# Kernel tuning notes

Hardware: AMD Instinct MI355X
Metric: run time of the kernel (lower is better)

## Reference

```python
import jax, jax.numpy as jnp
import numpy as np

N, M, C, MID, K = 131072, 4096, 32, 16, 6
BN_EPS = 1e-5


def _bn(x, g, b, mu, var):
    # eval-mode BatchNorm over channel (last) axis
    return g * (x - mu) * jax.lax.rsqrt(var + BN_EPS) + b


def _block(x, w1, b1, g, b, mu, var, w2, b2):
    # Conv1d(kernel_size=1) stack == per-position linear over channels
    h = jax.nn.relu(_bn(x @ w1.T + b1, g, b, mu, var))
    return h @ w2.T + b2


def _l2norm(x):
    # F.normalize(p=2, dim=channel) with eps=1e-12 clamp
    return x / jnp.maximum(jnp.linalg.norm(x, axis=-1, keepdims=True), 1e-12)


def _forward(sp_fea, sp_xyz, o_p_fea, p_xyz, idx_abs, idx_rel, params):
    (wf1_w, wf1_b, wf_g, wf_b, wf_m, wf_v, wf2_w, wf2_b,
     wx1_w, wx1_b, wx_g, wx_b, wx_m, wx_v, wx2_w, wx2_b,
     m1_w, m1_b, mb_g, mb_b, mb_m, mb_v, m2_w, m2_b) = params
    m = sp_fea.shape[1]
    c = o_p_fea.shape[1]
    # gather each point's K candidate superpoint fea/xyz, center on the point
    c2p_fea = sp_fea[0][idx_abs] - o_p_fea[:, None, :]   # (n, K, C)
    c2p_xyz = sp_xyz[0][idx_abs] - p_xyz[:, None, :]     # (n, K, 3)
    # point MLP: Linear -> BN -> ReLU -> Linear
    p_fea = jax.nn.relu(_bn(o_p_fea @ m1_w.T + m1_b, mb_g, mb_b, mb_m, mb_v)) @ m2_w.T + m2_b  # (n, C)
    w_fea = _block(c2p_fea, wf1_w, wf1_b, wf_g, wf_b, wf_m, wf_v, wf2_w, wf2_b)  # (n, K, C)
    w_xyz = _block(c2p_xyz, wx1_w, wx1_b, wx_g, wx_b, wx_m, wx_v, wx2_w, wx2_b)  # (n, K, C)
    p_fea, w_fea, w_xyz = _l2norm(p_fea), _l2norm(w_fea), _l2norm(w_xyz)
    # bilateral weights over the K candidates
    bi_w = jax.nn.softmax(
        jnp.einsum('nc,nkc->nk', p_fea, w_fea) * jnp.einsum('nc,nkc->nk', p_fea, w_xyz),
        axis=-1)  # (n, K)
    # weighted segment aggregation points -> superpoints
    # (equivalent to building the dense (m, n) association matrix f and matmul)
    ridx = idx_rel.reshape(-1)                                     # (n*K,)
    wsum = jax.ops.segment_sum(bi_w.reshape(-1), ridx, num_segments=m)  # (m,)
    agg_fea = jax.ops.segment_sum((bi_w[..., None] * o_p_fea[:, None, :]).reshape(-1, c), ridx, num_segments=m)
    agg_xyz = jax.ops.segment_sum((bi_w[..., None] * p_xyz[:, None, :]).reshape(-1, 3), ridx, num_segments=m)
    denom = wsum[:, None] + 1e-8
    return (agg_fea / denom)[None], (agg_xyz / denom)[None]  # (1, m, C), (1, m, 3)


def setup_inputs() -> dict:
    key = jax.random.key(0)
    ks = jax.random.split(key, 20)
    f32 = jnp.float32
    idx = jax.random.randint(ks[4], (1, N, K), 0, M, dtype=jnp.int32)
    inp = {
        'sp_fea': jax.random.normal(ks[0], (1, M, C), f32),
        'sp_xyz': jax.random.normal(ks[1], (1, M, 3), f32),
        'o_p_fea': jax.random.normal(ks[2], (N, C), f32),
        'p_xyz': jax.random.normal(ks[3], (N, 3), f32),
        'c2p_idx_abs': idx,
        'c2p_idx': idx,  # bs=1 -> absolute == relative indices
        'cluster_idx': jax.random.randint(ks[5], (N,), 0, M, dtype=jnp.int32),
        'offset': jnp.array([N], dtype=jnp.int32),
        'wf1_w': jax.random.normal(ks[6], (MID, C), f32) * 0.2,
        'wf1_b': jnp.zeros((MID,), f32),
        'wf_bn_g': jnp.ones((MID,), f32),
        'wf_bn_b': jnp.zeros((MID,), f32),
        'wf_bn_m': jax.random.normal(ks[7], (MID,), f32) * 0.1,
        'wf_bn_v': jax.random.uniform(ks[8], (MID,), f32, 0.5, 1.5),
        'wf2_w': jax.random.normal(ks[9], (C, MID), f32) * 0.2,
        'wf2_b': jnp.zeros((C,), f32),
        'wx1_w': jax.random.normal(ks[10], (MID, 3), f32) * 0.2,
        'wx1_b': jnp.zeros((MID,), f32),
        'wx_bn_g': jnp.ones((MID,), f32),
        'wx_bn_b': jnp.zeros((MID,), f32),
        'wx_bn_m': jax.random.normal(ks[11], (MID,), f32) * 0.1,
        'wx_bn_v': jax.random.uniform(ks[12], (MID,), f32, 0.5, 1.5),
        'wx2_w': jax.random.normal(ks[13], (C, MID), f32) * 0.2,
        'wx2_b': jnp.zeros((C,), f32),
        'mlp1_w': jax.random.normal(ks[14], (C, C), f32) * 0.2,
        'mlp1_b': jnp.zeros((C,), f32),
        'mlp_bn_g': jnp.ones((C,), f32),
        'mlp_bn_b': jnp.zeros((C,), f32),
        'mlp_bn_m': jax.random.normal(ks[15], (C,), f32) * 0.1,
        'mlp_bn_v': jax.random.uniform(ks[16], (C,), f32, 0.5, 1.5),
        'mlp2_w': jax.random.normal(ks[17], (C, C), f32) * 0.2,
        'mlp2_b': jnp.zeros((C,), f32),
    }
    return inp


def reference(sp_fea, sp_xyz, o_p_fea, p_xyz, c2p_idx_abs, c2p_idx, cluster_idx, offset,
              wf1_w, wf1_b, wf_bn_g, wf_bn_b, wf_bn_m, wf_bn_v, wf2_w, wf2_b,
              wx1_w, wx1_b, wx_bn_g, wx_bn_b, wx_bn_m, wx_bn_v, wx2_w, wx2_b,
              mlp1_w, mlp1_b, mlp_bn_g, mlp_bn_b, mlp_bn_m, mlp_bn_v, mlp2_w, mlp2_b):
    params = (wf1_w, wf1_b, wf_bn_g, wf_bn_b, wf_bn_m, wf_bn_v, wf2_w, wf2_b,
              wx1_w, wx1_b, wx_bn_g, wx_bn_b, wx_bn_m, wx_bn_v, wx2_w, wx2_b,
              mlp1_w, mlp1_b, mlp_bn_g, mlp_bn_b, mlp_bn_m, mlp_bn_v, mlp2_w, mlp2_b)
    return _forward(sp_fea, sp_xyz, o_p_fea, p_xyz, c2p_idx_abs[0], c2p_idx[0], params)
```

## Files before the change

kernel.cpp:

```cpp
#include <hip/hip_runtime.h>

#define M_ 4096
#define N_ 131072
#define K_ 6
#define C_ 32
#define MID_ 16
#define CAP_ 320
#define CNT_STRIDE 16
#define PB 32

#define OFF_AF 0
#define OFF_AX (M_*MID_)
#define OFF_CB (2*M_*MID_)
#define CB_WF1T 0
#define CB_WX1T 512
#define CB_M1T  576
#define CB_TM   1600
#define CB_QFMT 1632
#define CB_QXMT 2144
#define CB_QF0  2656
#define CB_QX0  2672
#define CB_G2   2688
#define CB_M2TB 3712
#define CB_PBFV 3744
#define CB_PBXV 3776
#define CB_GF   3808
#define CB_GX   4064
#define CB_VF   4320
#define CB_VX   4336
#define CB_SC   4352
#define CB_N    4360
#define OFF_CNT  (OFF_CB + CB_N + 8)
#define OFF_PAIR (OFF_CNT + M_*CNT_STRIDE)

#define BN_EPS 1e-5f

__global__ void prep_kernel(
    const float* __restrict__ sp_fea, const float* __restrict__ sp_xyz,
    const float* __restrict__ wf1_w, const float* __restrict__ wf1_b,
    const float* __restrict__ wf_g, const float* __restrict__ wf_b,
    const float* __restrict__ wf_m, const float* __restrict__ wf_v,
    const float* __restrict__ wf2_w, const float* __restrict__ wf2_b,
    const float* __restrict__ wx1_w, const float* __restrict__ wx1_b,
    const float* __restrict__ wx_g, const float* __restrict__ wx_b,
    const float* __restrict__ wx_m, const float* __restrict__ wx_v,
    const float* __restrict__ wx2_w, const float* __restrict__ wx2_b,
    const float* __restrict__ m1_w, const float* __restrict__ m1_b,
    const float* __restrict__ mb_g, const float* __restrict__ mb_b,
    const float* __restrict__ mb_m, const float* __restrict__ mb_v,
    const float* __restrict__ m2_w, const float* __restrict__ m2_b,
    float* __restrict__ ws)
{
    const int gid = blockIdx.x * blockDim.x + threadIdx.x;

    if (gid < M_) {
        float sp[32];
        #pragma unroll
        for (int q = 0; q < 8; ++q) {
            float4 v = *(const float4*)(sp_fea + gid*32 + 4*q);
            sp[4*q] = v.x; sp[4*q+1] = v.y; sp[4*q+2] = v.z; sp[4*q+3] = v.w;
        }
        #pragma unroll
        for (int j = 0; j < 16; ++j) {
            float s = wf_g[j] * rsqrtf(wf_v[j] + BN_EPS);
            float t = s * wf1_b[j] + wf_b[j] - s * wf_m[j];
            float acc = 0.f;
            #pragma unroll
            for (int c = 0; c < 32; ++c) acc += sp[c] * wf1_w[j*32 + c];
            ws[OFF_AF + gid*16 + j] = s * acc + t;
        }
        float sx0 = sp_xyz[gid*3], sx1 = sp_xyz[gid*3+1], sx2 = sp_xyz[gid*3+2];
        #pragma unroll
        for (int j = 0; j < 16; ++j) {
            float s = wx_g[j] * rsqrtf(wx_v[j] + BN_EPS);
            float t = s * wx1_b[j] + wx_b[j] - s * wx_m[j];
            float acc = sx0*wx1_w[j*3] + sx1*wx1_w[j*3+1] + sx2*wx1_w[j*3+2];
            ws[OFF_AX + gid*16 + j] = s * acc + t;
        }
    }

    if (blockIdx.x == 0) {
        const int t = threadIdx.x;
        float* cb = ws + OFF_CB;

        for (int e = t; e < 512; e += 256) {
            int c = e >> 4, jj = e & 15;
            float s = wf_g[jj] * rsqrtf(wf_v[jj] + BN_EPS);
            cb[CB_WF1T + e] = s * wf1_w[jj*32 + c];
            float aqf = 0.f, aqx = 0.f;
            #pragma unroll
            for (int i = 0; i < 32; ++i) {
                aqf += wf2_w[i*16 + jj] * m2_w[i*32 + c];
                aqx += wx2_w[i*16 + jj] * m2_w[i*32 + c];
            }
            cb[CB_QFMT + e] = aqf;
            cb[CB_QXMT + e] = aqx;
        }
        if (t < 64) {
            int c = t >> 4, jj = t & 15;
            float s = wx_g[jj] * rsqrtf(wx_v[jj] + BN_EPS);
            cb[CB_WX1T + t] = (c < 3) ? s * wx1_w[jj*3 + c] : 0.f;
        }
        for (int e = t; e < 1024; e += 256) {
            int c = e >> 5, i = e & 31;
            float s = mb_g[i] * rsqrtf(mb_v[i] + BN_EPS);
            cb[CB_M1T + e] = s * m1_w[i*32 + c];
            int q = e >> 5, p = e & 31;
            float a = 0.f;
            #pragma unroll
            for (int i2 = 0; i2 < 32; ++i2) a += m2_w[i2*32 + q] * m2_w[i2*32 + p];
            cb[CB_G2 + e] = a;
        }
        if (t < 32) {
            float s = mb_g[t] * rsqrtf(mb_v[t] + BN_EPS);
            cb[CB_TM + t] = s * m1_b[t] + mb_b[t] - s * mb_m[t];
            float a = 0.f, bf = 0.f, bx = 0.f;
            #pragma unroll
            for (int i2 = 0; i2 < 32; ++i2) {
                a  += m2_w[i2*32 + t] * m2_b[i2];
                bf += m2_w[i2*32 + t] * wf2_b[i2];
                bx += m2_w[i2*32 + t] * wx2_b[i2];
            }
            cb[CB_M2TB + t] = a;
            cb[CB_PBFV + t] = bf;
            cb[CB_PBXV + t] = bx;
        }
        if (t < 256) {
            int jj = t >> 4, p = t & 15;
            float accf = 0.f, accx = 0.f;
            #pragma unroll
            for (int i2 = 0; i2 < 32; ++i2) {
                accf += wf2_w[i2*16 + jj] * wf2_w[i2*16 + p];
                accx += wx2_w[i2*16 + jj] * wx2_w[i2*16 + p];
            }
            cb[CB_GF + t] = accf;
            cb[CB_GX + t] = accx;
        }
        if (t < 16) {
            float q0f = 0.f, q0x = 0.f, vf = 0.f, vx = 0.f;
            #pragma unroll
            for (int i2 = 0; i2 < 32; ++i2) {
                q0f += wf2_w[i2*16 + t] * m2_b[i2];
                q0x += wx2_w[i2*16 + t] * m2_b[i2];
                vf  += wf2_w[i2*16 + t] * wf2_b[i2];
                vx  += wx2_w[i2*16 + t] * wx2_b[i2];
            }
            cb[CB_QF0 + t] = q0f;
            cb[CB_QX0 + t] = q0x;
            cb[CB_VF + t] = vf;
            cb[CB_VX + t] = vx;
        }
        if (t == 0) {
            float bbf = 0.f, bbx = 0.f, bb2 = 0.f, pcf = 0.f, pcx = 0.f;
            #pragma unroll
            for (int i2 = 0; i2 < 32; ++i2) {
                bbf += wf2_b[i2]*wf2_b[i2];
                bbx += wx2_b[i2]*wx2_b[i2];
                bb2 += m2_b[i2]*m2_b[i2];
                pcf += m2_b[i2]*wf2_b[i2];
                pcx += m2_b[i2]*wx2_b[i2];
            }
            cb[CB_SC+0] = bbf; cb[CB_SC+1] = bbx; cb[CB_SC+2] = bb2;
            cb[CB_SC+3] = pcf; cb[CB_SC+4] = pcx;
            cb[CB_SC+5] = 0.f; cb[CB_SC+6] = 0.f; cb[CB_SC+7] = 0.f;
        }
    }
}

__global__ __launch_bounds__(256) void fused_kernel(
    const float* __restrict__ o_p_fea, const float* __restrict__ p_xyz,
    const int* __restrict__ idx_abs, float* __restrict__ ws)
{
    __shared__ float cb[CB_N];
    __shared__ float opl[PB*33];
    __shared__ float hpb[PB*36];
    __shared__ float pkl[PB*72];

    const int tid = threadIdx.x;
    const int base = blockIdx.x * PB;
    {
        const float* src = ws + OFF_CB;
        for (int i = tid; i < CB_N; i += 256) cb[i] = src[i];
        #pragma unroll
        for (int u = 0; u < 4; ++u) {
            const int idx = tid + u*256;
            opl[(idx >> 5)*33 + (idx & 31)] = o_p_fea[(size_t)base*32 + idx];
        }
    }
    __syncthreads();

    const int g = tid >> 4;
    const int j = tid & 15;
    const int n0 = base + 2*g;
    const int n1 = n0 + 1;

    float af0=0.f, af1=0.f, h00=0.f, h01=0.f, h10=0.f, h11=0.f;
    #pragma unroll
    for (int c = 0; c < 32; ++c) {
        const float op0 = opl[(2*g)*33 + c];
        const float op1 = opl[(2*g+1)*33 + c];
        const float w   = cb[CB_WF1T + c*16 + j];
        const float m0  = cb[CB_M1T + c*32 + 2*j];
        const float m1v = cb[CB_M1T + c*32 + 2*j + 1];
        af0 += w*op0;  af1 += w*op1;
        h00 += m0*op0; h01 += m1v*op0;
        h10 += m0*op1; h11 += m1v*op1;
    }
    {
        const float tm0 = cb[CB_TM + 2*j], tm1 = cb[CB_TM + 2*j + 1];
        h00 = fmaxf(h00 + tm0, 0.f); h01 = fmaxf(h01 + tm1, 0.f);
        h10 = fmaxf(h10 + tm0, 0.f); h11 = fmaxf(h11 + tm1, 0.f);
    }
    const float wx0 = cb[CB_WX1T + j], wx1v = cb[CB_WX1T + 16 + j], wx2v = cb[CB_WX1T + 32 + j];
    const float ax0 = wx0*p_xyz[n0*3] + wx1v*p_xyz[n0*3+1] + wx2v*p_xyz[n0*3+2];
    const float ax1 = wx0*p_xyz[n1*3] + wx1v*p_xyz[n1*3+1] + wx2v*p_xyz[n1*3+2];

    hpb[(2*g)*36 + 2*j]       = h00;
    hpb[(2*g)*36 + 2*j + 1]   = h01;
    hpb[(2*g+1)*36 + 2*j]     = h10;
    hpb[(2*g+1)*36 + 2*j + 1] = h11;
    __syncthreads();

    const float q0i = cb[CB_QF0 + j], qx0i = cb[CB_QX0 + j];
    float qf0 = q0i, qf1 = q0i, qx0 = qx0i, qx1 = qx0i;
    float t200=0.f, t201=0.f, t210=0.f, t211=0.f;
    #pragma unroll
    for (int q = 0; q < 32; ++q) {
        const float hq0 = hpb[(2*g)*36 + q];
        const float hq1 = hpb[(2*g+1)*36 + q];
        const float wqf = cb[CB_QFMT + q*16 + j];
        const float wqx = cb[CB_QXMT + q*16 + j];
        const float ga  = cb[CB_G2 + q*32 + 2*j];
        const float gb  = cb[CB_G2 + q*32 + 2*j + 1];
        qf0 += wqf*hq0; qf1 += wqf*hq1;
        qx0 += wqx*hq0; qx1 += wqx*hq1;
        t200 += ga*hq0; t201 += gb*hq0;
        t210 += ga*hq1; t211 += gb*hq1;
    }
    const float m2tb0 = 2.f*cb[CB_M2TB + 2*j], m2tb1 = 2.f*cb[CB_M2TB + 2*j + 1];
    const float pbv0 = cb[CB_PBFV + 2*j], pbv1 = cb[CB_PBFV + 2*j + 1];
    const float pxv0 = cb[CB_PBXV + 2*j], pxv1 = cb[CB_PBXV + 2*j + 1];
    float pn20 = h00*(t200 + m2tb0) + h01*(t201 + m2tb1);
    float pn21 = h10*(t210 + m2tb0) + h11*(t211 + m2tb1);
    float pbf0 = h00*pbv0 + h01*pbv1;
    float pbf1 = h10*pbv0 + h11*pbv1;
    float pbx0 = h00*pxv0 + h01*pxv1;
    float pbx1 = h10*pxv0 + h11*pxv1;
    #pragma unroll
    for (int mm = 1; mm < 16; mm <<= 1) {
        pn20 += __shfl_xor(pn20, mm, 16);
        pn21 += __shfl_xor(pn21, mm, 16);
        pbf0 += __shfl_xor(pbf0, mm, 16);
        pbf1 += __shfl_xor(pbf1, mm, 16);
        pbx0 += __shfl_xor(pbx0, mm, 16);
        pbx1 += __shfl_xor(pbx1, mm, 16);
    }
    const float sc2v = cb[CB_SC + 2], sc3v = cb[CB_SC + 3], sc4v = cb[CB_SC + 4];
    const float inv0 = 1.0f / fmaxf(sqrtf(fmaxf(pn20 + sc2v, 0.f)), 1e-12f);
    const float inv1 = 1.0f / fmaxf(sqrtf(fmaxf(pn21 + sc2v, 0.f)), 1e-12f);

    ((float4*)(pkl + (2*g)*72))[j]   = make_float4(af0, ax0, qf0*inv0, qx0*inv0);
    ((float4*)(pkl + (2*g+1)*72))[j] = make_float4(af1, ax1, qf1*inv1, qx1*inv1);
    if (j == 0) {
        pkl[(2*g)*72 + 64]   = (pbf0 + sc3v) * inv0;
        pkl[(2*g)*72 + 65]   = (pbx0 + sc4v) * inv0;
        pkl[(2*g+1)*72 + 64] = (pbf1 + sc3v) * inv1;
        pkl[(2*g+1)*72 + 65] = (pbx1 + sc4v) * inv1;
    }
    __syncthreads();

    const int slot = tid >> 3;
    const int k    = tid & 7;
    const int n    = base + slot;
    const int kc   = (k < K_) ? k : (K_ - 1);
    const int r    = idx_abs[n * K_ + kc];
    const float* pkb = pkl + slot*72;

    float afr[16], axr[16];
    #pragma unroll
    for (int q4 = 0; q4 < 4; ++q4) {
        float4 a = *(const float4*)(ws + OFF_AF + r*16 + 4*q4);
        float4 b = *(const float4*)(ws + OFF_AX + r*16 + 4*q4);
        afr[4*q4] = a.x; afr[4*q4+1] = a.y; afr[4*q4+2] = a.z; afr[4*q4+3] = a.w;
        axr[4*q4] = b.x; axr[4*q4+1] = b.y; axr[4*q4+2] = b.z; axr[4*q4+3] = b.w;
    }

    float hf[16], hx[16];
    float df = 0.f, dx = 0.f, nf2 = 0.f, nx2 = 0.f;
    #pragma unroll
    for (int jj = 0; jj < 16; ++jj) {
        const float4 v4 = ((const float4*)pkb)[jj];
        const float h1 = fmaxf(afr[jj] - v4.x, 0.f);
        const float h2 = fmaxf(axr[jj] - v4.y, 0.f);
        hf[jj] = h1; hx[jj] = h2;
        df  += v4.z * h1;
        dx  += v4.w * h2;
        nf2 += cb[CB_VF + jj] * h1;
        nx2 += cb[CB_VX + jj] * h2;
    }
    const float scbx = pkb[64], scby = pkb[65];

    float nfq = 0.f, nxq = 0.f;
    #pragma unroll
    for (int q = 0; q < 16; ++q) {
        float sf = 0.f, sx = 0.f;
        #pragma unroll
        for (int p4 = 0; p4 < 4; ++p4) {
            const float4 gf = *(const float4*)&cb[CB_GF + q*16 + 4*p4];
            const float4 gx = *(const float4*)&cb[CB_GX + q*16 + 4*p4];
            sf += gf.x*hf[4*p4] + gf.y*hf[4*p4+1] + gf.z*hf[4*p4+2] + gf.w*hf[4*p4+3];
            sx += gx.x*hx[4*p4] + gx.y*hx[4*p4+1] + gx.z*hx[4*p4+2] + gx.w*hx[4*p4+3];
        }
        nfq += hf[q] * sf;
        nxq += hx[q] * sx;
    }
    const float nf = fmaxf(nfq + 2.f*nf2 + cb[CB_SC + 0], 0.f);
    const float nx = fmaxf(nxq + 2.f*nx2 + cb[CB_SC + 1], 0.f);
    const float invf = 1.0f / fmaxf(sqrtf(nf), 1e-12f);
    const float invx = 1.0f / fmaxf(sqrtf(nx), 1e-12f);
    float logit = ((df + scbx) * invf) * ((dx + scby) * invx);
    if (k >= K_) logit = -3.0e38f;

    float mx = logit;
    mx = fmaxf(mx, __shfl_xor(mx, 1));
    mx = fmaxf(mx, __shfl_xor(mx, 2));
    mx = fmaxf(mx, __shfl_xor(mx, 4));
    float ex = __expf(logit - mx);
    float s = ex;
    s += __shfl_xor(s, 1);
    s += __shfl_xor(s, 2);
    s += __shfl_xor(s, 4);
    const float w = ex / s;

    if (k < K_) {
        int*  cnt   = (int*)(ws + OFF_CNT);
        int2* pairs = (int2*)(ws + OFF_PAIR);
        const int pos = atomicAdd(&cnt[r*CNT_STRIDE], 1);
        if (pos < CAP_) {
            pairs[(size_t)r*CAP_ + pos] = make_int2(n, __float_as_int(w));
        }
    }
}

__global__ __launch_bounds__(256) void agg_kernel(
    const float* __restrict__ ws,
    const float* __restrict__ o_p_fea, const float* __restrict__ p_xyz,
    float* __restrict__ out)
{
    __shared__ float red[4][40];

    const int wave = threadIdx.x >> 6;
    const int lane = threadIdx.x & 63;
    const int m = blockIdx.x;
    const int eo = lane >> 5;
    const int c  = lane & 31;

    const int*  cnt   = (const int*)(ws + OFF_CNT);
    const int2* pairs = (const int2*)(ws + OFF_PAIR);

    int cn = cnt[m*CNT_STRIDE];
    if (cn > CAP_) cn = CAP_;
    const int2* pb = pairs + (size_t)m * CAP_;

    float acc = 0.f, wacc = 0.f, xacc = 0.f;
    for (int e2 = (wave*2 + eo)*2; e2 < cn; e2 += 16) {
        const int4 pq = *(const int4*)&pb[e2];
        {
            const int nn  = pq.x;
            const float w = __int_as_float(pq.y);
            acc += w * o_p_fea[(size_t)nn*32 + c];
            if (c == 0) wacc += w;
            if (c < 3)  xacc += w * p_xyz[nn*3 + c];
        }
        if (e2 + 1 < cn) {
            const int nn  = pq.z;
            const float w = __int_as_float(pq.w);
            acc += w * o_p_fea[(size_t)nn*32 + c];
            if (c == 0) wacc += w;
            if (c < 3)  xacc += w * p_xyz[nn*3 + c];
        }
    }
    acc  += __shfl_xor(acc, 32);
    xacc += __shfl_xor(xacc, 32);
    wacc += __shfl_xor(wacc, 32);
    if (eo == 0) {
        red[wave][c] = acc;
        if (c < 3)  red[wave][33 + c] = xacc;
        if (c == 0) red[wave][36] = wacc;
    }
    __syncthreads();

    if (wave == 0 && eo == 0) {
        const float a = red[0][c] + red[1][c] + red[2][c] + red[3][c];
        const float wtot = red[0][36] + red[1][36] + red[2][36] + red[3][36];
        const float denom = wtot + 1e-8f;
        out[m*32 + c] = a / denom;
        if (c < 3) {
            const float x = red[0][33+c] + red[1][33+c] + red[2][33+c] + red[3][33+c];
            out[M_*C_ + m*3 + c] = x / denom;
        }
    }
}

extern "C" void kernel_launch(void* const* d_in, const int* in_sizes, int n_in,
                              void* d_out, int out_size, void* d_ws, size_t ws_size,
                              hipStream_t stream)
{
    const float* sp_fea  = (const float*)d_in[0];
    const float* sp_xyz  = (const float*)d_in[1];
    const float* o_p_fea = (const float*)d_in[2];
    const float* p_xyz   = (const float*)d_in[3];
    const int*   idx_abs = (const int*)d_in[4];
    const float* wf1_w = (const float*)d_in[8];
    const float* wf1_b = (const float*)d_in[9];
    const float* wf_g  = (const float*)d_in[10];
    const float* wf_b  = (const float*)d_in[11];
    const float* wf_m  = (const float*)d_in[12];
    const float* wf_v  = (const float*)d_in[13];
    const float* wf2_w = (const float*)d_in[14];
    const float* wf2_b = (const float*)d_in[15];
    const float* wx1_w = (const float*)d_in[16];
    const float* wx1_b = (const float*)d_in[17];
    const float* wx_g  = (const float*)d_in[18];
    const float* wx_b  = (const float*)d_in[19];
    const float* wx_m  = (const float*)d_in[20];
    const float* wx_v  = (const float*)d_in[21];
    const float* wx2_w = (const float*)d_in[22];
    const float* wx2_b = (const float*)d_in[23];
    const float* m1_w  = (const float*)d_in[24];
    const float* m1_b  = (const float*)d_in[25];
    const float* mb_g  = (const float*)d_in[26];
    const float* mb_b  = (const float*)d_in[27];
    const float* mb_m  = (const float*)d_in[28];
    const float* mb_v  = (const float*)d_in[29];
    const float* m2_w  = (const float*)d_in[30];
    const float* m2_b  = (const float*)d_in[31];

    float* ws = (float*)d_ws;
    float* out = (float*)d_out;

    hipMemsetAsync(ws + OFF_CNT, 0, (size_t)(M_*CNT_STRIDE) * sizeof(int), stream);

    prep_kernel<<<16, 256, 0, stream>>>(
        sp_fea, sp_xyz,
        wf1_w, wf1_b, wf_g, wf_b, wf_m, wf_v, wf2_w, wf2_b,
        wx1_w, wx1_b, wx_g, wx_b, wx_m, wx_v, wx2_w, wx2_b,
        m1_w, m1_b, mb_g, mb_b, mb_m, mb_v, m2_w, m2_b,
        ws);

    fused_kernel<<<N_/PB, 256, 0, stream>>>(o_p_fea, p_xyz, idx_abs, ws);

    agg_kernel<<<M_, 256, 0, stream>>>(ws, o_p_fea, p_xyz, out);
}
```

Measured before the change: 136.2 us.

## Replace Gram quadratic form with Cholesky-factored triangular norm computation

Precomputes a Cholesky factor of the second-layer Gram matrices in the prep kernel and solves for a linear term, so the per-candidate squared norm becomes a sum of squares of an upper-triangular matvec plus a constant. This roughly halves the inner quadratic-form FLOPs and removes the separate linear-term accumulation. It also overlays the shared-memory buffers for point features and the packed per-point data, shrinking LDS use per block at the cost of an extra barrier. The factorization relies on the Gram matrix being positive definite and clamps tiny pivots, which may change numerics slightly.

```diff
diff --git a/kernel.cpp b/kernel.cpp
--- a/kernel.cpp
+++ b/kernel.cpp
@@ -8,6 +8,7 @@
 #define CAP_ 320
 #define CNT_STRIDE 16
 #define PB 32
+#define PKS 68
 
 #define OFF_AF 0
 #define OFF_AX (M_*MID_)
@@ -24,10 +25,10 @@
 #define CB_M2TB 3712
 #define CB_PBFV 3744
 #define CB_PBXV 3776
-#define CB_GF   3808
-#define CB_GX   4064
-#define CB_VF   4320
-#define CB_VX   4336
+#define CB_UF   3808
+#define CB_UX   4064
+#define CB_CF   4320
+#define CB_CX   4336
 #define CB_SC   4352
 #define CB_N    4360
 #define OFF_CNT  (OFF_CB + CB_N + 8)
@@ -80,6 +81,8 @@
     }
 
     if (blockIdx.x == 0) {
+        __shared__ float sG[512];
+        __shared__ float svv[40];
         const int t = threadIdx.x;
         float* cb = ws + OFF_CB;
 
@@ -125,7 +128,7 @@
             cb[CB_PBFV + t] = bf;
             cb[CB_PBXV + t] = bx;
         }
-        if (t < 256) {
+        {
             int jj = t >> 4, p = t & 15;
             float accf = 0.f, accx = 0.f;
             #pragma unroll
@@ -133,8 +136,8 @@
                 accf += wf2_w[i2*16 + jj] * wf2_w[i2*16 + p];
                 accx += wx2_w[i2*16 + jj] * wx2_w[i2*16 + p];
             }
-            cb[CB_GF + t] = accf;
-            cb[CB_GX + t] = accx;
+            sG[t]       = accf;
+            sG[256 + t] = accx;
         }
         if (t < 16) {
             float q0f = 0.f, q0x = 0.f, vf = 0.f, vx = 0.f;
@@ -147,8 +150,8 @@
             }
             cb[CB_QF0 + t] = q0f;
             cb[CB_QX0 + t] = q0x;
-            cb[CB_VF + t] = vf;
-            cb[CB_VX + t] = vx;
+            svv[t]      = vf;
+            svv[16 + t] = vx;
         }
         if (t == 0) {
             float bbf = 0.f, bbx = 0.f, bb2 = 0.f, pcf = 0.f, pcx = 0.f;
@@ -160,9 +163,59 @@
                 pcf += m2_b[i2]*wf2_b[i2];
                 pcx += m2_b[i2]*wx2_b[i2];
             }
-            cb[CB_SC+0] = bbf; cb[CB_SC+1] = bbx; cb[CB_SC+2] = bb2;
+            svv[32] = bbf; svv[33] = bbx;
+            cb[CB_SC+2] = bb2;
             cb[CB_SC+3] = pcf; cb[CB_SC+4] = pcx;
             cb[CB_SC+5] = 0.f; cb[CB_SC+6] = 0.f; cb[CB_SC+7] = 0.f;
+        }
+        __syncthreads();
+
+        if (t < 64) {
+            const int lane = t;
+            const int half = lane >> 5;
+            const int p    = lane & 31;
+            const bool act = (p < 16);
+            const int pp   = p & 15;
+            const int sb   = half ? 32 : 0;
+
+            float c[16];
+            #pragma unroll
+            for (int k = 0; k < 16; ++k)
+                c[k] = act ? sG[half*256 + k*16 + pp] : 0.f;
+
+            float u[16];
+            #pragma unroll
+            for (int k = 0; k < 16; ++k) {
+                const float gkk = __shfl(c[k], sb + k);
+                const float d = sqrtf(fmaxf(gkk, 1e-30f));
+                const float ukp = c[k] / d;
+                u[k] = ukp;
+                #pragma unroll
+                for (int j2 = k + 1; j2 < 16; ++j2)
+                    c[j2] -= __shfl(ukp, sb + j2) * ukp;
+            }
+
+            const float v = act ? svv[half*16 + pp] : 0.f;
+            float acc = 0.f, cf = 0.f;
+            #pragma unroll
+            for (int i = 0; i < 16; ++i) {
+                const float cand = (v - acc) / u[i];
+                const float ci = __shfl(cand, sb + i);
+                if (pp == i) cf = ci;
+                acc += ((i <= pp) ? u[i] : 0.f) * ci;
+            }
+            float s2 = act ? cf * cf : 0.f;
+            s2 += __shfl_xor(s2, 1); s2 += __shfl_xor(s2, 2);
+            s2 += __shfl_xor(s2, 4); s2 += __shfl_xor(s2, 8);
+
+            if (act) {
+                float* dst = ws + OFF_CB + (half ? CB_UX : CB_UF);
+                #pragma unroll
+                for (int k = 0; k < 16; ++k)
+                    dst[k*16 + pp] = (k <= pp) ? u[k] : 0.f;
+                ws[OFF_CB + (half ? CB_CX : CB_CF) + pp] = cf;
+                if (pp == 0) ws[OFF_CB + CB_SC + half] = svv[32 + half] - s2;
+            }
         }
     }
 }
@@ -172,9 +225,10 @@
     const int* __restrict__ idx_abs, float* __restrict__ ws)
 {
     __shared__ float cb[CB_N];
-    __shared__ float opl[PB*33];
-    __shared__ float hpb[PB*36];
-    __shared__ float pkl[PB*72];
+    __shared__ float ovl[PB*33 + PB*36];
+    float* opl = ovl;
+    float* hpb = ovl + PB*33;
+    float* pkl = ovl;
 
     const int tid = threadIdx.x;
     const int base = blockIdx.x * PB;
@@ -259,13 +313,15 @@
     const float inv0 = 1.0f / fmaxf(sqrtf(fmaxf(pn20 + sc2v, 0.f)), 1e-12f);
     const float inv1 = 1.0f / fmaxf(sqrtf(fmaxf(pn21 + sc2v, 0.f)), 1e-12f);
 
-    ((float4*)(pkl + (2*g)*72))[j]   = make_float4(af0, ax0, qf0*inv0, qx0*inv0);
-    ((float4*)(pkl + (2*g+1)*72))[j] = make_float4(af1, ax1, qf1*inv1, qx1*inv1);
+    __syncthreads();
+
+    ((float4*)(pkl + (2*g)*PKS))[j]   = make_float4(af0, ax0, qf0*inv0, qx0*inv0);
+    ((float4*)(pkl + (2*g+1)*PKS))[j] = make_float4(af1, ax1, qf1*inv1, qx1*inv1);
     if (j == 0) {
-        pkl[(2*g)*72 + 64]   = (pbf0 + sc3v) * inv0;
-        pkl[(2*g)*72 + 65]   = (pbx0 + sc4v) * inv0;
-        pkl[(2*g+1)*72 + 64] = (pbf1 + sc3v) * inv1;
-        pkl[(2*g+1)*72 + 65] = (pbx1 + sc4v) * inv1;
+        pkl[(2*g)*PKS + 64]   = (pbf0 + sc3v) * inv0;
+        pkl[(2*g)*PKS + 65]   = (pbx0 + sc4v) * inv0;
+        pkl[(2*g+1)*PKS + 64] = (pbf1 + sc3v) * inv1;
+        pkl[(2*g+1)*PKS + 65] = (pbx1 + sc4v) * inv1;
     }
     __syncthreads();
 
@@ -274,7 +330,7 @@
     const int n    = base + slot;
     const int kc   = (k < K_) ? k : (K_ - 1);
     const int r    = idx_abs[n * K_ + kc];
-    const float* pkb = pkl + slot*72;
+    const float* pkb = pkl + slot*PKS;
 
     float afr[16], axr[16];
     #pragma unroll
@@ -286,38 +342,35 @@
     }
 
     float hf[16], hx[16];
-    float df = 0.f, dx = 0.f, nf2 = 0.f, nx2 = 0.f;
+    float df = 0.f, dx = 0.f;
     #pragma unroll
     for (int jj = 0; jj < 16; ++jj) {
         const float4 v4 = ((const float4*)pkb)[jj];
         const float h1 = fmaxf(afr[jj] - v4.x, 0.f);
         const float h2 = fmaxf(axr[jj] - v4.y, 0.f);
         hf[jj] = h1; hx[jj] = h2;
-        df  += v4.z * h1;
-        dx  += v4.w * h2;
-        nf2 += cb[CB_VF + jj] * h1;
-        nx2 += cb[CB_VX + jj] * h2;
+        df += v4.z * h1;
+        dx += v4.w * h2;
     }
     const float scbx = pkb[64], scby = pkb[65];
 
-    float nfq = 0.f, nxq = 0.f;
+    float nf = cb[CB_SC + 0], nx = cb[CB_SC + 1];
     #pragma unroll
     for (int q = 0; q < 16; ++q) {
-        float sf = 0.f, sx = 0.f;
+        float yf = cb[CB_CF + q];
+        float yx = cb[CB_CX + q];
         #pragma unroll
-        for (int p4 = 0; p4 < 4; ++p4) {
-            const float4 gf = *(const float4*)&cb[CB_GF + q*16 + 4*p4];
-            const float4 gx = *(const float4*)&cb[CB_GX + q*16 + 4*p4];
-            sf += gf.x*hf[4*p4] + gf.y*hf[4*p4+1] + gf.z*hf[4*p4+2] + gf.w*hf[4*p4+3];
-            sx += gx.x*hx[4*p4] + gx.y*hx[4*p4+1] + gx.z*hx[4*p4+2] + gx.w*hx[4*p4+3];
-        }
-        nfq += hf[q] * sf;
-        nxq += hx[q] * sx;
-    }
-    const float nf = fmaxf(nfq + 2.f*nf2 + cb[CB_SC + 0], 0.f);
-    const float nx = fmaxf(nxq + 2.f*nx2 + cb[CB_SC + 1], 0.f);
-    const float invf = 1.0f / fmaxf(sqrtf(nf), 1e-12f);
-    const float invx = 1.0f / fmaxf(sqrtf(nx), 1e-12f);
+        for (int p4 = (q >> 2); p4 < 4; ++p4) {
+            const float4 uf = *(const float4*)&cb[CB_UF + q*16 + 4*p4];
+            const float4 ux = *(const float4*)&cb[CB_UX + q*16 + 4*p4];
+            yf += uf.x*hf[4*p4] + uf.y*hf[4*p4+1] + uf.z*hf[4*p4+2] + uf.w*hf[4*p4+3];
+            yx += ux.x*hx[4*p4] + ux.y*hx[4*p4+1] + ux.z*hx[4*p4+2] + ux.w*hx[4*p4+3];
+        }
+        nf += yf * yf;
+        nx += yx * yx;
+    }
+    const float invf = 1.0f / fmaxf(sqrtf(fmaxf(nf, 0.f)), 1e-12f);
+    const float invx = 1.0f / fmaxf(sqrtf(fmaxf(nx, 0.f)), 1e-12f);
     float logit = ((df + scbx) * invf) * ((dx + scby) * invx);
     if (k >= K_) logit = -3.0e38f;
 
```

After: 132.7 us. 2.6% less time.
